# Kernel tuning notes

Measured on AMD Instinct MI355X. Metric: run time of the kernel, lower is better.

## Reference

```python
import jax, jax.numpy as jnp
import numpy as np

DET = 512       # detector bins
N_THETA = 180   # projection angles, theta = 0..179 degrees (1 deg spacing)


def _ramp_filter(size):
    """skimage _get_fourier_filter(size, 'ramp'): spatial ramp -> FFT."""
    n = np.concatenate((np.arange(1, size // 2 + 1, 2),
                        np.arange(size // 2 - 1, 0, -2)))
    f = np.zeros(size)
    f[0] = 0.25
    f[1::2] = -1.0 / (np.pi * n) ** 2
    return jnp.asarray(2.0 * np.real(np.fft.fft(f)), dtype=jnp.float32)


def _iradon(x):
    B, C, det, A = x.shape
    theta = jnp.deg2rad(jnp.arange(A, dtype=jnp.float32))  # 0..179 deg

    # --- ramp filtering along the detector axis ---
    size = max(64, int(2 ** np.ceil(np.log2(2 * det))))  # 1024 for det=512
    filt = _ramp_filter(size)                            # (size,)
    xp = jnp.pad(x, ((0, 0), (0, 0), (0, size - det), (0, 0)))
    proj_f = jnp.fft.fft(xp, axis=2) * filt[None, None, :, None]
    filtered = jnp.real(jnp.fft.ifft(proj_f, axis=2))[:, :, :det, :]  # (B,C,det,A)

    # --- backprojection (circle=False) ---
    out_size = int(np.floor(np.sqrt(det ** 2 / 2.0)))  # 362
    radius = out_size // 2
    xpr = jnp.arange(out_size, dtype=jnp.float32)[:, None] - radius  # rows
    ypr = jnp.arange(out_size, dtype=jnp.float32)[None, :] - radius  # cols
    cos_t = jnp.cos(theta)
    sin_t = jnp.sin(theta)
    # detector coordinate for every (angle, pixel): t = y*cos - x*sin
    t = ypr[None] * cos_t[:, None, None] - xpr[None] * sin_t[:, None, None]  # (A,out,out)
    pos = t + det // 2          # index into detector axis (x = arange(det)-det//2)
    i0 = jnp.floor(pos).astype(jnp.int32)
    frac = pos - i0.astype(jnp.float32)
    in_range = ((pos >= 0) & (pos <= det - 1)).astype(jnp.float32)  # fill_value=0 outside
    i0c = jnp.clip(i0, 0, det - 1)
    i1c = jnp.clip(i0 + 1, 0, det - 1)

    P = out_size * out_size
    ft = jnp.moveaxis(filtered, 3, 2)                     # (B,C,A,det)
    idx0 = jnp.broadcast_to(i0c.reshape(A, P)[None, None], (B, C, A, P))
    idx1 = jnp.broadcast_to(i1c.reshape(A, P)[None, None], (B, C, A, P))
    g0 = jnp.take_along_axis(ft, idx0, axis=3)            # (B,C,A,P)
    g1 = jnp.take_along_axis(ft, idx1, axis=3)
    w = frac.reshape(A, P)[None, None]
    m = in_range.reshape(A, P)[None, None]
    val = ((1.0 - w) * g0 + w * g1) * m                   # bilinear-in-1D interp, 0 outside
    recon = val.sum(axis=2).reshape(B, C, out_size, out_size)
    return recon * (jnp.pi / (2.0 * A))


def setup_inputs() -> dict:
    key = jax.random.key(0)
    x = jax.random.normal(key, (4, 1, DET, N_THETA), dtype=jnp.float32)
    return {"x": x}


def reference(x):
    return _iradon(x)
```

## Files before the change

kernel.cpp:

```cpp
#include <hip/hip_runtime.h>
#include <math.h>

#define DET 512
#define NA  180
#define OUT 362
#define RAD 181

#define NSPLIT 3
#define APB    60
#define CHUNK  10
#define LSTRIDE 516

constexpr double PI_D = 3.14159265358979323846;

constexpr double tsin(double x) {
    double x2 = x * x;
    return x * (1.0 + x2 * (-1.0/6 + x2 * (1.0/120 + x2 * (-1.0/5040 +
               x2 * (1.0/362880 + x2 * (-1.0/39916800))))));
}
constexpr double tcos(double x) {
    double x2 = x * x;
    return 1.0 + x2 * (-0.5 + x2 * (1.0/24 + x2 * (-1.0/720 +
               x2 * (1.0/40320 + x2 * (-1.0/3628800)))));
}

struct Trig { float c[NA]; float s[NA]; };
constexpr Trig make_trig() {
    Trig t{};
    constexpr double r = PI_D / 180.0;
    for (int k = 0; k < NA; ++k) {
        double c, s;
        if (k <= 45)       { c =  tcos(k * r);          s =  tsin(k * r); }
        else if (k <= 90)  { c =  tsin((90 - k) * r);   s =  tcos((90 - k) * r); }
        else if (k <= 135) { c = -tsin((k - 90) * r);   s =  tcos((k - 90) * r); }
        else               { c = -tcos((180 - k) * r);  s =  tsin((180 - k) * r); }
        t.c[k] = (float)c; t.s[k] = (float)s;
    }
    return t;
}
__device__ constexpr Trig TRIG = make_trig();

struct WTbl { float w[DET / 2]; };
constexpr WTbl make_wt() {
    WTbl t{};
    for (int k = 0; k < DET / 2; ++k) {
        double m = (double)(2 * k + 1);
        t.w[k] = (float)(-2.0 / (PI_D * PI_D * m * m));
    }
    return t;
}
__device__ constexpr WTbl WTC = make_wt();

__global__ __launch_bounds__(512) void ramp_filter_kernel(
        const float* __restrict__ x, float* __restrict__ ft) {
    const int a = blockIdx.x;
    const int b = blockIdx.y;
    const int tid = threadIdx.x;

    __shared__ float xs[3 * DET];

    xs[tid]        = 0.0f;
    xs[1024 + tid] = 0.0f;
    xs[512 + tid]  = x[(b * DET + tid) * NA + a];
    __syncthreads();

    const float* p = xs + 512 + tid;
    float acc = 0.5f * p[0];
    #pragma unroll 4
    for (int k = 0; k < DET / 2; ++k) {
        int m = 2 * k + 1;
        acc = fmaf(WTC.w[k], p[-m] + p[m], acc);
    }
    ft[(b * NA + a) * DET + tid] = acc;
}

__device__ __forceinline__ float interp1(const float* __restrict__ L, float pos) {
    float pf = floorf(pos);
    int   i0 = (int)pf;
    float fr = pos - pf;
    float g0 = L[i0];
    float g1 = L[i0 + 1];
    float v  = fmaf(fr, g1 - g0, g0);
    return pos <= (float)(DET - 1) ? v : 0.0f;
}

__global__ __launch_bounds__(256) void backproject_kernel(
        const float* __restrict__ ft, float* __restrict__ out) {
    const int bz = blockIdx.z;
    const int b  = bz / NSPLIT;
    const int sp = bz - b * NSPLIT;
    const int r0 = blockIdx.y * 32;
    const int c0 = blockIdx.x * 32;
    const int tid = threadIdx.x;
    const int tx = tid & 15;
    const int ty = tid >> 4;

    __shared__ float line[CHUNK * LSTRIDE];

    if (tid < CHUNK) line[tid * LSTRIDE + 512] = 0.0f;

    const float xpr = (float)(min(r0 + ty, OUT - 1) - RAD);
    const float ypr = (float)(min(c0 + tx, OUT - 1) - RAD);

    float a00 = 0.0f, a01 = 0.0f, a10 = 0.0f, a11 = 0.0f;

    const float* base = ft + (b * NA + sp * APB) * DET;

    for (int rd = 0; rd < APB / CHUNK; ++rd) {
        __syncthreads();
        const float4* g = (const float4*)(base + rd * CHUNK * DET);
        #pragma unroll
        for (int k = 0; k < (CHUNK * DET / 4) / 256; ++k) {
            int j4 = tid + k * 256;
            float4 v = g[j4];
            int c = j4 >> 7;
            int d = (j4 & 127) << 2;
            *(float4*)&line[c * LSTRIDE + d] = v;
        }
        __syncthreads();

        const int abase = sp * APB + rd * CHUNK;
        #pragma unroll
        for (int i = 0; i < CHUNK; ++i) {
            const float cv = TRIG.c[abase + i];
            const float sv = TRIG.s[abase + i];
            float p00 = fmaf(ypr, cv, fmaf(xpr, -sv, 256.0f));
            float p01 = fmaf(16.0f, cv, p00);
            float p10 = fmaf(-16.0f, sv, p00);
            float p11 = fmaf(-16.0f, sv, p01);
            const float* L = line + i * LSTRIDE;
            a00 += interp1(L, p00);
            a01 += interp1(L, p01);
            a10 += interp1(L, p10);
            a11 += interp1(L, p11);
        }
    }

    const float scale = (float)(PI_D / (2.0 * NA));
    const int r = r0 + ty;
    const int c = c0 + tx;
    float* ob = out + b * OUT * OUT;
    if (r < OUT) {
        if (c < OUT)      atomicAdd(&ob[r * OUT + c],      a00 * scale);
        if (c + 16 < OUT) atomicAdd(&ob[r * OUT + c + 16], a01 * scale);
    }
    if (r + 16 < OUT) {
        if (c < OUT)      atomicAdd(&ob[(r + 16) * OUT + c],      a10 * scale);
        if (c + 16 < OUT) atomicAdd(&ob[(r + 16) * OUT + c + 16], a11 * scale);
    }
}

extern "C" void kernel_launch(void* const* d_in, const int* in_sizes, int n_in,
                              void* d_out, int out_size, void* d_ws, size_t ws_size,
                              hipStream_t stream) {
    const float* x = (const float*)d_in[0];
    float* ft  = (float*)d_ws;
    float* out = (float*)d_out;

    const int B = in_sizes[0] / (DET * NA);

    hipMemsetAsync(out, 0, (size_t)out_size * sizeof(float), stream);
    ramp_filter_kernel<<<dim3(NA, B), 512, 0, stream>>>(x, ft);
    backproject_kernel<<<dim3((OUT + 31) / 32, (OUT + 31) / 32, B * NSPLIT),
                         256, 0, stream>>>(ft, out);
}
```

Baseline: 104.9 us.

## Register-block ramp filter convolution and fold output zeroing into filter kernel

```diff
diff --git a/kernel.cpp b/kernel.cpp
--- a/kernel.cpp
+++ b/kernel.cpp
@@ -40,38 +40,82 @@
 }
 __device__ constexpr Trig TRIG = make_trig();
 
-struct WTbl { float w[DET / 2]; };
-constexpr WTbl make_wt() {
-    WTbl t{};
-    for (int k = 0; k < DET / 2; ++k) {
-        double m = (double)(2 * k + 1);
-        t.w[k] = (float)(-2.0 / (PI_D * PI_D * m * m));
-    }
+struct WTab { float w[2][127][8]; };
+constexpr WTab make_wtab() {
+    WTab t{};
+    for (int h = 0; h < 2; ++h)
+        for (int ui = 0; ui < 127; ++ui)
+            for (int di = 0; di < 8; ++di) {
+                int m = 8 * (ui - 63) + 2 * (di - 3) - 1 + 2 * h;
+                double md = (double)m;
+                t.w[h][ui][di] = (float)(-2.0 / (PI_D * PI_D * md * md));
+            }
     return t;
 }
-__device__ constexpr WTbl WTC = make_wt();
-
-__global__ __launch_bounds__(512) void ramp_filter_kernel(
-        const float* __restrict__ x, float* __restrict__ ft) {
+__device__ constexpr WTab WTAB = make_wtab();
+
+__global__ __launch_bounds__(128) void ramp_filter_kernel(
+        const float* __restrict__ x, float* __restrict__ ft,
+        float* __restrict__ out, int n4, int pb4) {
     const int a = blockIdx.x;
     const int b = blockIdx.y;
-    const int tid = threadIdx.x;
-
-    __shared__ float xs[3 * DET];
-
-    xs[tid]        = 0.0f;
-    xs[1024 + tid] = 0.0f;
-    xs[512 + tid]  = x[(b * DET + tid) * NA + a];
+    const int t = threadIdx.x;
+
+    {
+        float4* oz = (float4*)out;
+        const float4 z4 = make_float4(0.f, 0.f, 0.f, 0.f);
+        const int base4 = (b * NA + a) * pb4;
+        for (int i = t; i < pb4; i += 128) {
+            int idx = base4 + i;
+            if (idx < n4) oz[idx] = z4;
+        }
+    }
+
+    __shared__ float Ef[768];
+    __shared__ float Of[768];
+
+    const float2 z2 = make_float2(0.f, 0.f);
+    *(float2*)&Ef[2 * t]       = z2;
+    *(float2*)&Ef[512 + 2 * t] = z2;
+    *(float2*)&Of[2 * t]       = z2;
+    *(float2*)&Of[512 + 2 * t] = z2;
+
+    const float* xc = x + (size_t)(b * DET) * NA + a;
+    float v0 = xc[(4 * t + 0) * NA];
+    float v1 = xc[(4 * t + 1) * NA];
+    float v2 = xc[(4 * t + 2) * NA];
+    float v3 = xc[(4 * t + 3) * NA];
+    *(float2*)&Ef[256 + 2 * t] = make_float2(v0, v2);
+    *(float2*)&Of[256 + 2 * t] = make_float2(v1, v3);
     __syncthreads();
 
-    const float* p = xs + 512 + tid;
-    float acc = 0.5f * p[0];
+    const int half = t >> 6;
+    const int tp   = t & 63;
+    const float4* src4  = (const float4*)(half ? Ef : Of);
+    const float4* self4 = (const float4*)(half ? Of : Ef);
+
+    float acc0 = 0.f, acc1 = 0.f, acc2 = 0.f, acc3 = 0.f;
     #pragma unroll 4
-    for (int k = 0; k < DET / 2; ++k) {
-        int m = 2 * k + 1;
-        acc = fmaf(WTC.w[k], p[-m] + p[m], acc);
-    }
-    ft[(b * NA + a) * DET + tid] = acc;
+    for (int ui = 0; ui < 127; ++ui) {
+        const float* __restrict__ w = WTAB.w[half][ui];
+        float4 s4 = src4[tp + (127 - ui)];
+        acc0 = fmaf(s4.x, w[3], fmaf(s4.y, w[2], fmaf(s4.z, w[1], fmaf(s4.w, w[0], acc0))));
+        acc1 = fmaf(s4.x, w[4], fmaf(s4.y, w[3], fmaf(s4.z, w[2], fmaf(s4.w, w[1], acc1))));
+        acc2 = fmaf(s4.x, w[5], fmaf(s4.y, w[4], fmaf(s4.z, w[3], fmaf(s4.w, w[2], acc2))));
+        acc3 = fmaf(s4.x, w[6], fmaf(s4.y, w[5], fmaf(s4.z, w[4], fmaf(s4.w, w[3], acc3))));
+    }
+
+    float4 sf = self4[64 + tp];
+    acc0 = fmaf(0.5f, sf.x, acc0);
+    acc1 = fmaf(0.5f, sf.y, acc1);
+    acc2 = fmaf(0.5f, sf.z, acc2);
+    acc3 = fmaf(0.5f, sf.w, acc3);
+
+    float* o = ft + (b * NA + a) * DET + 8 * tp + half;
+    o[0] = acc0;
+    o[2] = acc1;
+    o[4] = acc2;
+    o[6] = acc3;
 }
 
 __device__ __forceinline__ float interp1(const float* __restrict__ L, float pos) {
@@ -159,8 +203,10 @@
 
     const int B = in_sizes[0] / (DET * NA);
 
-    hipMemsetAsync(out, 0, (size_t)out_size * sizeof(float), stream);
-    ramp_filter_kernel<<<dim3(NA, B), 512, 0, stream>>>(x, ft);
+    const int n4  = out_size / 4;
+    const int pb4 = (n4 + NA * B - 1) / (NA * B);
+
+    ramp_filter_kernel<<<dim3(NA, B), 128, 0, stream>>>(x, ft, out, n4, pb4);
     backproject_kernel<<<dim3((OUT + 31) / 32, (OUT + 31) / 32, B * NSPLIT),
                          256, 0, stream>>>(ft, out);
 }
```

Result: slower. 113.3 us (+8.0%).
